# Optimization experiments

Measured on AMD Instinct MI355X. Metric: run time of the kernel, lower is better.

## Reference

```python
import jax, jax.numpy as jnp
import numpy as np


def setup_inputs() -> dict:
    key = jax.random.key(0)
    ks = jax.random.split(key, 6)
    b, t, s, qu, vu, d = 8, 64, 512, 512, 512, 512
    return {
        "query": jax.random.normal(ks[0], (b, t, qu), jnp.float32),
        "value": jax.random.normal(ks[1], (b, s, vu), jnp.float32),
        "mask": jax.random.randint(ks[2], (b, s), 0, 2).astype(bool),
        "W1_w": jax.random.normal(ks[3], (qu, d), jnp.float32) * (1.0 / np.sqrt(qu)),
        "W1_b": jnp.zeros((d,), jnp.float32),
        "W2_w": jax.random.normal(ks[4], (vu, d), jnp.float32) * (1.0 / np.sqrt(vu)),
        "W2_b": jnp.zeros((d,), jnp.float32),
        "scale": jax.random.normal(ks[5], (d,), jnp.float32) * 0.05,
    }


def reference(query, value, mask, W1_w, W1_b, W2_w, W2_b, scale):
    # Dense projections
    q = jnp.einsum('btq,qd->btd', query, W1_w) + W1_b   # [b,t,d]
    k = jnp.einsum('bsv,vd->bsd', value, W2_w) + W2_b   # [b,s,d]
    # Additive (Bahdanau) score with learned scale vector (Keras use_scale=True)
    # scores[b,t,s] = sum_d scale[d] * tanh(q[b,t,d] + k[b,s,d])
    scores = jnp.einsum('btsd,d->bts', jnp.tanh(q[:, :, None, :] + k[:, None, :, :]), scale)
    # Mask over source positions (value mask); query mask is all-ones (no-op)
    scores = jnp.where(mask[:, None, :], scores, jnp.float32(-1e9))
    attention_weights = jax.nn.softmax(scores, axis=-1)   # [b,t,s]
    context_vector = jnp.einsum('bts,bsv->btv', attention_weights, value)  # [b,t,vu]
    return context_vector, attention_weights
```

## Files before the change

kernel.cpp:

```cpp
#include <hip/hip_runtime.h>
#include <hip/hip_bf16.h>

#define B_  8
#define T_  64
#define S_  512
#define D_  512

#define QN (512 * 512)
#define KN (4096 * 512)
#define SN (B_ * T_ * S_)

#define TLOG2E 2.8853900817779268f
#define LOG2E  1.4426950408889634f

typedef __attribute__((ext_vector_type(8))) short bf16x8;
typedef __attribute__((ext_vector_type(4))) float f32x4;

__device__ __forceinline__ unsigned short f2bf(float f) {
    unsigned int u = __float_as_uint(f);
    return (unsigned short)((u + 0x7FFFu + ((u >> 16) & 1u)) >> 16);
}
__device__ __forceinline__ unsigned int pk2(float a, float b) {
    return (unsigned int)f2bf(a) | ((unsigned int)f2bf(b) << 16);
}

__global__ __launch_bounds__(256) void pack_bf16(
    const float* __restrict__ query, const float* __restrict__ value,
    const float* __restrict__ W1, const float* __restrict__ W2,
    unsigned short* __restrict__ qb, unsigned short* __restrict__ vb,
    unsigned short* __restrict__ w1t, unsigned short* __restrict__ w2t)
{
    const int blk = blockIdx.x;
    const int tid = threadIdx.x;
    if (blk < 1152) {
        const float* src; unsigned short* dst; int lb;
        if (blk < 1024) { src = value; dst = vb; lb = blk; }
        else            { src = query; dst = qb; lb = blk - 1024; }
        size_t o = (size_t)lb * 2048 + tid * 8;
        float4 x = *(const float4*)(src + o);
        float4 y = *(const float4*)(src + o + 4);
        uint4 p;
        p.x = pk2(x.x, x.y); p.y = pk2(x.z, x.w);
        p.z = pk2(y.x, y.y); p.w = pk2(y.z, y.w);
        *(uint4*)(dst + o) = p;
    } else {
        const float* W; unsigned short* Wt; int lb;
        if (blk < 1280) { W = W1; Wt = w1t; lb = blk - 1152; }
        else            { W = W2; Wt = w2t; lb = blk - 1280; }
        size_t o = (size_t)lb * 2048 + tid * 8;
        const int n  = (int)(o >> 9);
        const int k0 = (int)(o & 511);
        uint4 p;
        p.x = pk2(W[(size_t)(k0 + 0) * 512 + n], W[(size_t)(k0 + 1) * 512 + n]);
        p.y = pk2(W[(size_t)(k0 + 2) * 512 + n], W[(size_t)(k0 + 3) * 512 + n]);
        p.z = pk2(W[(size_t)(k0 + 4) * 512 + n], W[(size_t)(k0 + 5) * 512 + n]);
        p.w = pk2(W[(size_t)(k0 + 6) * 512 + n], W[(size_t)(k0 + 7) * 512 + n]);
        *(uint4*)(Wt + o) = p;
    }
}

__global__ __launch_bounds__(256) void mfma_gemm(
    const unsigned short* __restrict__ qb, const unsigned short* __restrict__ vb,
    const unsigned short* __restrict__ w1t, const unsigned short* __restrict__ w2t,
    const float* __restrict__ b1, const float* __restrict__ b2,
    float* __restrict__ qproj, float* __restrict__ kproj)
{
    __shared__ __align__(16) unsigned short Ab[64][40];
    __shared__ __align__(16) unsigned short Bb[64][40];

    const int x = blockIdx.x;
    const unsigned short *A, *Bt;
    float* C;
    int tm, tn;
    bool isq;
    if (x < 512) {
        tm = x >> 3; tn = x & 7;
        A = vb; Bt = w2t; C = kproj; isq = false;
    } else {
        int r = x - 512;
        tm = r >> 3; tn = r & 7;
        A = qb; Bt = w1t; C = qproj; isq = true;
    }

    const int tid  = threadIdx.x;
    const int lane = tid & 63;
    const int wid  = tid >> 6;
    const int wm = (wid & 1) * 32, wn = (wid >> 1) * 32;
    const int fm = lane & 15, fq = lane >> 4;

    f32x4 acc00 = {0.f, 0.f, 0.f, 0.f};
    f32x4 acc01 = acc00, acc10 = acc00, acc11 = acc00;

    const int ar = tid >> 2;
    const int ac = (tid & 3) * 8;
    const unsigned short* Ag = A  + (size_t)(tm * 64 + ar) * 512 + ac;
    const unsigned short* Bg = Bt + (size_t)(tn * 64 + ar) * 512 + ac;

    for (int k0 = 0; k0 < 512; k0 += 32) {
        *(uint4*)&Ab[ar][ac] = *(const uint4*)(Ag + k0);
        *(uint4*)&Bb[ar][ac] = *(const uint4*)(Bg + k0);
        __syncthreads();
        bf16x8 a0 = *(const bf16x8*)&Ab[wm + fm][fq * 8];
        bf16x8 a1 = *(const bf16x8*)&Ab[wm + 16 + fm][fq * 8];
        bf16x8 b0 = *(const bf16x8*)&Bb[wn + fm][fq * 8];
        bf16x8 b1v = *(const bf16x8*)&Bb[wn + 16 + fm][fq * 8];
        acc00 = __builtin_amdgcn_mfma_f32_16x16x32_bf16(a0, b0,  acc00, 0, 0, 0);
        acc01 = __builtin_amdgcn_mfma_f32_16x16x32_bf16(a0, b1v, acc01, 0, 0, 0);
        acc10 = __builtin_amdgcn_mfma_f32_16x16x32_bf16(a1, b0,  acc10, 0, 0, 0);
        acc11 = __builtin_amdgcn_mfma_f32_16x16x32_bf16(a1, b1v, acc11, 0, 0, 0);
        __syncthreads();
    }

    const int n0 = tn * 64 + wn + fm;
    const int n1 = n0 + 16;
    float bias0 = 0.f, bias1 = 0.f;
    if (isq) {
        bias0 = b1[n0] + b2[n0];
        bias1 = b1[n1] + b2[n1];
    }
    const int m0 = tm * 64 + wm + fq * 4;
#pragma unroll
    for (int r = 0; r < 4; ++r) {
        C[(size_t)(m0 + r) * 512 + n0]      = (acc00[r] + bias0) * TLOG2E;
        C[(size_t)(m0 + r) * 512 + n1]      = (acc01[r] + bias1) * TLOG2E;
        C[(size_t)(m0 + 16 + r) * 512 + n0] = (acc10[r] + bias0) * TLOG2E;
        C[(size_t)(m0 + 16 + r) * 512 + n1] = (acc11[r] + bias1) * TLOG2E;
    }
}

__global__ __launch_bounds__(256, 4) void scores_t(
    const float* __restrict__ qproj, const float* __restrict__ kproj,
    const int*   __restrict__ mask,  const float* __restrict__ scale,
    float* __restrict__ sparts)
{
    const int blk = blockIdx.x;
    const int b  = blk & 7;
    int r = blk >> 3;
    const int dh = r & 1;
    r >>= 1;
    const int sg = r & 31;
    const int tg = r >> 5;
    const int t0 = tg * 16, s0 = sg * 16;
    const int dbase = dh * 256;

    __shared__ float kT[16][132];
    __shared__ float qT[16][132];
    __shared__ float cS[128];

    const int tid  = threadIdx.x;
    const int t_l = tid >> 4;
    const int s_l = tid & 15;
    const int m = mask[b * S_ + s0 + s_l];

    const int lrow = tid >> 5;
    const int lcol = (tid & 31) * 4;

    float p0 = 0.f, p1 = 0.f;

    for (int c = 0; c < 2; ++c) {
        const int dc = dbase + c * 128;
        const float* kp = kproj + (size_t)(b * S_ + s0) * D_ + dc;
        const float* qp = qproj + (size_t)(b * T_ + t0) * D_ + dc;
        *(float4*)&kT[lrow][lcol]     = *(const float4*)(kp + (size_t)lrow * D_ + lcol);
        *(float4*)&kT[lrow + 8][lcol] = *(const float4*)(kp + (size_t)(lrow + 8) * D_ + lcol);
        *(float4*)&qT[lrow][lcol]     = *(const float4*)(qp + (size_t)lrow * D_ + lcol);
        *(float4*)&qT[lrow + 8][lcol] = *(const float4*)(qp + (size_t)(lrow + 8) * D_ + lcol);
        if (tid < 32) {
            *(float4*)&cS[tid * 4] = *(const float4*)(scale + dc + tid * 4);
        }
        __syncthreads();

#pragma unroll 4
        for (int j = 0; j < 32; ++j) {
            float4 k4 = *(const float4*)&kT[s_l][j * 4];
            float4 q4 = *(const float4*)&qT[t_l][j * 4];
            float4 c4 = *(const float4*)&cS[j * 4];
            float e0 = __builtin_amdgcn_exp2f(q4.x + k4.x);
            float e1 = __builtin_amdgcn_exp2f(q4.y + k4.y);
            float e2 = __builtin_amdgcn_exp2f(q4.z + k4.z);
            float e3 = __builtin_amdgcn_exp2f(q4.w + k4.w);
            float r0 = __builtin_amdgcn_rcpf(e0 + 1.0f);
            float r1 = __builtin_amdgcn_rcpf(e1 + 1.0f);
            float r2 = __builtin_amdgcn_rcpf(e2 + 1.0f);
            float r3 = __builtin_amdgcn_rcpf(e3 + 1.0f);
            p0 = fmaf(c4.x, r0, p0);
            p1 = fmaf(c4.y, r1, p1);
            p0 = fmaf(c4.z, r2, p0);
            p1 = fmaf(c4.w, r3, p1);
        }
        __syncthreads();
    }

    const float p = p0 + p1;
    const float out = m ? (-2.0f * p) : -5e8f;
    sparts[(size_t)dh * SN + (size_t)(b * T_ + t0 + t_l) * S_ + s0 + s_l] = out;
}

__global__ __launch_bounds__(256) void softmax_ctx(
    const float* __restrict__ sparts, const float* __restrict__ value,
    float* __restrict__ ctx, float* __restrict__ attn)
{
    const int blk = blockIdx.x;
    const int b = blk & 7;
    int r = blk >> 3;
    const int vc = r & 3;
    const int tp = r >> 2;
    const int t0 = tp * 2, t1 = t0 + 1;
    const size_t row0 = (size_t)(b * T_ + t0) * S_;
    const size_t row1 = row0 + S_;

    const int tid  = threadIdx.x;
    const int lane = tid & 63;
    const int wid  = tid >> 6;

    __shared__ float2 wp[S_];
    __shared__ float4 part[2][8][32];
    __shared__ float2 red2[8];

    const int sa = tid, sb = tid + 256;
    float2 xa, xb;
    xa.x = sparts[row0 + sa] + sparts[SN + row0 + sa];
    xa.y = sparts[row1 + sa] + sparts[SN + row1 + sa];
    xb.x = sparts[row0 + sb] + sparts[SN + row0 + sb];
    xb.y = sparts[row1 + sb] + sparts[SN + row1 + sb];

    float2 m2; m2.x = fmaxf(xa.x, xb.x); m2.y = fmaxf(xa.y, xb.y);
#pragma unroll
    for (int off = 32; off >= 1; off >>= 1) {
        m2.x = fmaxf(m2.x, __shfl_xor(m2.x, off));
        m2.y = fmaxf(m2.y, __shfl_xor(m2.y, off));
    }
    if (lane == 0) red2[wid] = m2;
    __syncthreads();
    {
        float2 r0 = red2[0], r1 = red2[1], r2 = red2[2], r3 = red2[3];
        m2.x = fmaxf(fmaxf(r0.x, r1.x), fmaxf(r2.x, r3.x));
        m2.y = fmaxf(fmaxf(r0.y, r1.y), fmaxf(r2.y, r3.y));
    }

    float2 ea, eb;
    ea.x = __builtin_amdgcn_exp2f((xa.x - m2.x) * LOG2E);
    ea.y = __builtin_amdgcn_exp2f((xa.y - m2.y) * LOG2E);
    eb.x = __builtin_amdgcn_exp2f((xb.x - m2.x) * LOG2E);
    eb.y = __builtin_amdgcn_exp2f((xb.y - m2.y) * LOG2E);

    float2 s2; s2.x = ea.x + eb.x; s2.y = ea.y + eb.y;
#pragma unroll
    for (int off = 32; off >= 1; off >>= 1) {
        s2.x += __shfl_xor(s2.x, off);
        s2.y += __shfl_xor(s2.y, off);
    }
    if (lane == 0) red2[4 + wid] = s2;
    __syncthreads();
    {
        float2 r0 = red2[4], r1 = red2[5], r2 = red2[6], r3 = red2[7];
        s2.x = (r0.x + r1.x) + (r2.x + r3.x);
        s2.y = (r0.y + r1.y) + (r2.y + r3.y);
    }
    const float inv0 = 1.0f / s2.x, inv1 = 1.0f / s2.y;

    float wa0 = ea.x * inv0, wb0 = eb.x * inv0;
    float wa1 = ea.y * inv1, wb1 = eb.y * inv1;

    float2 wsa; wsa.x = wa0; wsa.y = wa1;
    float2 wsb; wsb.x = wb0; wsb.y = wb1;
    wp[sa] = wsa;
    wp[sb] = wsb;
    if (vc == 0) {
        attn[row0 + sa] = wa0; attn[row0 + sb] = wb0;
        attn[row1 + sa] = wa1; attn[row1 + sb] = wb1;
    }
    __syncthreads();

    const int ssub = wid * 2 + (lane >> 5);
    const int v4   = lane & 31;
    const int v    = vc * 128 + v4 * 4;
    const float* vb = value + ((size_t)(b * S_) + ssub * 64) * D_ + v;
    float4 a0; a0.x = 0.f; a0.y = 0.f; a0.z = 0.f; a0.w = 0.f;
    float4 a1 = a0;
#pragma unroll 4
    for (int i = 0; i < 64; ++i) {
        float4 vv = *(const float4*)(vb + (size_t)i * D_);
        float2 w2 = wp[ssub * 64 + i];
        a0.x = fmaf(w2.x, vv.x, a0.x);
        a0.y = fmaf(w2.x, vv.y, a0.y);
        a0.z = fmaf(w2.x, vv.z, a0.z);
        a0.w = fmaf(w2.x, vv.w, a0.w);
        a1.x = fmaf(w2.y, vv.x, a1.x);
        a1.y = fmaf(w2.y, vv.y, a1.y);
        a1.z = fmaf(w2.y, vv.z, a1.z);
        a1.w = fmaf(w2.y, vv.w, a1.w);
    }
    part[0][ssub][v4] = a0;
    part[1][ssub][v4] = a1;
    __syncthreads();
    if (tid < 64) {
        const int ts = tid >> 5, w4 = tid & 31;
        float4 s0 = part[ts][0][w4], s1 = part[ts][1][w4];
        float4 s2v = part[ts][2][w4], s3 = part[ts][3][w4];
        float4 s4 = part[ts][4][w4], s5 = part[ts][5][w4];
        float4 s6 = part[ts][6][w4], s7 = part[ts][7][w4];
        float4 o;
        o.x = ((s0.x + s1.x) + (s2v.x + s3.x)) + ((s4.x + s5.x) + (s6.x + s7.x));
        o.y = ((s0.y + s1.y) + (s2v.y + s3.y)) + ((s4.y + s5.y) + (s6.y + s7.y));
        o.z = ((s0.z + s1.z) + (s2v.z + s3.z)) + ((s4.z + s5.z) + (s6.z + s7.z));
        o.w = ((s0.w + s1.w) + (s2v.w + s3.w)) + ((s4.w + s5.w) + (s6.w + s7.w));
        *(float4*)(ctx + (size_t)(b * T_ + t0 + ts) * D_ + vc * 128 + w4 * 4) = o;
    }
}

extern "C" void kernel_launch(void* const* d_in, const int* in_sizes, int n_in,
                              void* d_out, int out_size, void* d_ws, size_t ws_size,
                              hipStream_t stream) {
    const float* query = (const float*)d_in[0];
    const float* value = (const float*)d_in[1];
    const int*   mask  = (const int*)  d_in[2];
    const float* W1w   = (const float*)d_in[3];
    const float* W1b   = (const float*)d_in[4];
    const float* W2w   = (const float*)d_in[5];
    const float* W2b   = (const float*)d_in[6];
    const float* scale = (const float*)d_in[7];

    float* ctx  = (float*)d_out;
    float* attn = (float*)d_out + (size_t)B_ * T_ * D_;

    unsigned short* vb  = (unsigned short*)d_ws;
    unsigned short* qb  = vb + (size_t)KN;
    unsigned short* w1t = qb + (size_t)QN;
    unsigned short* w2t = w1t + (size_t)QN;
    float* qproj = (float*)(w2t + (size_t)QN);
    float* kproj = qproj + (size_t)QN;
    float* spart = kproj + (size_t)KN;

    pack_bf16<<<1408, 256, 0, stream>>>(query, value, W1w, W2w, qb, vb, w1t, w2t);
    mfma_gemm<<<576, 256, 0, stream>>>(qb, vb, w1t, w2t, W1b, W2b, qproj, kproj);
    scores_t<<<2048, 256, 0, stream>>>(qproj, kproj, mask, scale, spart);
    softmax_ctx<<<1024, 256, 0, stream>>>(spart, value, ctx, attn);
}
```

Measured before the change: 135.4 us.

## Fuse bf16 packing into GEMM with register prefetch; widen softmax to four rows

```diff
diff --git a/kernel.cpp b/kernel.cpp
--- a/kernel.cpp
+++ b/kernel.cpp
@@ -24,62 +24,28 @@
     return (unsigned int)f2bf(a) | ((unsigned int)f2bf(b) << 16);
 }
 
-__global__ __launch_bounds__(256) void pack_bf16(
+__global__ __launch_bounds__(256) void mfma_gemm(
     const float* __restrict__ query, const float* __restrict__ value,
     const float* __restrict__ W1, const float* __restrict__ W2,
-    unsigned short* __restrict__ qb, unsigned short* __restrict__ vb,
-    unsigned short* __restrict__ w1t, unsigned short* __restrict__ w2t)
-{
-    const int blk = blockIdx.x;
-    const int tid = threadIdx.x;
-    if (blk < 1152) {
-        const float* src; unsigned short* dst; int lb;
-        if (blk < 1024) { src = value; dst = vb; lb = blk; }
-        else            { src = query; dst = qb; lb = blk - 1024; }
-        size_t o = (size_t)lb * 2048 + tid * 8;
-        float4 x = *(const float4*)(src + o);
-        float4 y = *(const float4*)(src + o + 4);
-        uint4 p;
-        p.x = pk2(x.x, x.y); p.y = pk2(x.z, x.w);
-        p.z = pk2(y.x, y.y); p.w = pk2(y.z, y.w);
-        *(uint4*)(dst + o) = p;
-    } else {
-        const float* W; unsigned short* Wt; int lb;
-        if (blk < 1280) { W = W1; Wt = w1t; lb = blk - 1152; }
-        else            { W = W2; Wt = w2t; lb = blk - 1280; }
-        size_t o = (size_t)lb * 2048 + tid * 8;
-        const int n  = (int)(o >> 9);
-        const int k0 = (int)(o & 511);
-        uint4 p;
-        p.x = pk2(W[(size_t)(k0 + 0) * 512 + n], W[(size_t)(k0 + 1) * 512 + n]);
-        p.y = pk2(W[(size_t)(k0 + 2) * 512 + n], W[(size_t)(k0 + 3) * 512 + n]);
-        p.z = pk2(W[(size_t)(k0 + 4) * 512 + n], W[(size_t)(k0 + 5) * 512 + n]);
-        p.w = pk2(W[(size_t)(k0 + 6) * 512 + n], W[(size_t)(k0 + 7) * 512 + n]);
-        *(uint4*)(Wt + o) = p;
-    }
-}
-
-__global__ __launch_bounds__(256) void mfma_gemm(
-    const unsigned short* __restrict__ qb, const unsigned short* __restrict__ vb,
-    const unsigned short* __restrict__ w1t, const unsigned short* __restrict__ w2t,
     const float* __restrict__ b1, const float* __restrict__ b2,
     float* __restrict__ qproj, float* __restrict__ kproj)
 {
     __shared__ __align__(16) unsigned short Ab[64][40];
-    __shared__ __align__(16) unsigned short Bb[64][40];
+    __shared__ __align__(16) unsigned short Bs[64][40];
 
     const int x = blockIdx.x;
-    const unsigned short *A, *Bt;
+    const float *A, *W;
     float* C;
     int tm, tn;
     bool isq;
     if (x < 512) {
-        tm = x >> 3; tn = x & 7;
-        A = vb; Bt = w2t; C = kproj; isq = false;
+        tm = (x & 7) * 8 + ((x >> 3) & 7);
+        tn = x >> 6;
+        A = value; W = W2; C = kproj; isq = false;
     } else {
         int r = x - 512;
         tm = r >> 3; tn = r & 7;
-        A = qb; Bt = w1t; C = qproj; isq = true;
+        A = query; W = W1; C = qproj; isq = true;
     }
 
     const int tid  = threadIdx.x;
@@ -93,22 +59,43 @@
 
     const int ar = tid >> 2;
     const int ac = (tid & 3) * 8;
-    const unsigned short* Ag = A  + (size_t)(tm * 64 + ar) * 512 + ac;
-    const unsigned short* Bg = Bt + (size_t)(tn * 64 + ar) * 512 + ac;
+    const float* Ag = A + (size_t)(tm * 64 + ar) * 512 + ac;
+    const int c0 = (tid & 15) * 4;
+    const int kp = (tid >> 4) * 2;
+    const float* Wg = W + (size_t)kp * 512 + tn * 64 + c0;
+
+    float4 av0 = *(const float4*)(Ag);
+    float4 av1 = *(const float4*)(Ag + 4);
+    float4 wv0 = *(const float4*)(Wg);
+    float4 wv1 = *(const float4*)(Wg + 512);
 
     for (int k0 = 0; k0 < 512; k0 += 32) {
-        *(uint4*)&Ab[ar][ac] = *(const uint4*)(Ag + k0);
-        *(uint4*)&Bb[ar][ac] = *(const uint4*)(Bg + k0);
         __syncthreads();
-        bf16x8 a0 = *(const bf16x8*)&Ab[wm + fm][fq * 8];
-        bf16x8 a1 = *(const bf16x8*)&Ab[wm + 16 + fm][fq * 8];
-        bf16x8 b0 = *(const bf16x8*)&Bb[wn + fm][fq * 8];
-        bf16x8 b1v = *(const bf16x8*)&Bb[wn + 16 + fm][fq * 8];
+        {
+            uint4 pa;
+            pa.x = pk2(av0.x, av0.y); pa.y = pk2(av0.z, av0.w);
+            pa.z = pk2(av1.x, av1.y); pa.w = pk2(av1.z, av1.w);
+            *(uint4*)&Ab[ar][ac] = pa;
+            *(unsigned int*)&Bs[c0 + 0][kp] = pk2(wv0.x, wv1.x);
+            *(unsigned int*)&Bs[c0 + 1][kp] = pk2(wv0.y, wv1.y);
+            *(unsigned int*)&Bs[c0 + 2][kp] = pk2(wv0.z, wv1.z);
+            *(unsigned int*)&Bs[c0 + 3][kp] = pk2(wv0.w, wv1.w);
+        }
+        __syncthreads();
+        const int kn = (k0 + 32) & 511;
+        av0 = *(const float4*)(Ag + kn);
+        av1 = *(const float4*)(Ag + kn + 4);
+        wv0 = *(const float4*)(Wg + (size_t)kn * 512);
+        wv1 = *(const float4*)(Wg + (size_t)kn * 512 + 512);
+
+        bf16x8 a0  = *(const bf16x8*)&Ab[wm + fm][fq * 8];
+        bf16x8 a1  = *(const bf16x8*)&Ab[wm + 16 + fm][fq * 8];
+        bf16x8 b0  = *(const bf16x8*)&Bs[wn + fm][fq * 8];
+        bf16x8 b1v = *(const bf16x8*)&Bs[wn + 16 + fm][fq * 8];
         acc00 = __builtin_amdgcn_mfma_f32_16x16x32_bf16(a0, b0,  acc00, 0, 0, 0);
         acc01 = __builtin_amdgcn_mfma_f32_16x16x32_bf16(a0, b1v, acc01, 0, 0, 0);
         acc10 = __builtin_amdgcn_mfma_f32_16x16x32_bf16(a1, b0,  acc10, 0, 0, 0);
         acc11 = __builtin_amdgcn_mfma_f32_16x16x32_bf16(a1, b1v, acc11, 0, 0, 0);
-        __syncthreads();
     }
 
     const int n0 = tn * 64 + wn + fm;
@@ -204,71 +191,95 @@
     const int b = blk & 7;
     int r = blk >> 3;
     const int vc = r & 3;
-    const int tp = r >> 2;
-    const int t0 = tp * 2, t1 = t0 + 1;
-    const size_t row0 = (size_t)(b * T_ + t0) * S_;
-    const size_t row1 = row0 + S_;
+    const int tq = r >> 2;
+    const int t0 = tq * 4;
+    const size_t rbase = (size_t)(b * T_ + t0) * S_;
 
     const int tid  = threadIdx.x;
     const int lane = tid & 63;
     const int wid  = tid >> 6;
 
-    __shared__ float2 wp[S_];
-    __shared__ float4 part[2][8][32];
-    __shared__ float2 red2[8];
+    __shared__ float4 wp4[S_];
+    __shared__ float4 part[4][8][32];
+    __shared__ float4 red4[8];
 
     const int sa = tid, sb = tid + 256;
-    float2 xa, xb;
-    xa.x = sparts[row0 + sa] + sparts[SN + row0 + sa];
-    xa.y = sparts[row1 + sa] + sparts[SN + row1 + sa];
-    xb.x = sparts[row0 + sb] + sparts[SN + row0 + sb];
-    xb.y = sparts[row1 + sb] + sparts[SN + row1 + sb];
-
-    float2 m2; m2.x = fmaxf(xa.x, xb.x); m2.y = fmaxf(xa.y, xb.y);
+    float4 xa, xb;
+    xa.x = sparts[rbase + sa]          + sparts[SN + rbase + sa];
+    xa.y = sparts[rbase + S_ + sa]     + sparts[SN + rbase + S_ + sa];
+    xa.z = sparts[rbase + 2 * S_ + sa] + sparts[SN + rbase + 2 * S_ + sa];
+    xa.w = sparts[rbase + 3 * S_ + sa] + sparts[SN + rbase + 3 * S_ + sa];
+    xb.x = sparts[rbase + sb]          + sparts[SN + rbase + sb];
+    xb.y = sparts[rbase + S_ + sb]     + sparts[SN + rbase + S_ + sb];
+    xb.z = sparts[rbase + 2 * S_ + sb] + sparts[SN + rbase + 2 * S_ + sb];
+    xb.w = sparts[rbase + 3 * S_ + sb] + sparts[SN + rbase + 3 * S_ + sb];
+
+    float4 m4;
+    m4.x = fmaxf(xa.x, xb.x); m4.y = fmaxf(xa.y, xb.y);
+    m4.z = fmaxf(xa.z, xb.z); m4.w = fmaxf(xa.w, xb.w);
 #pragma unroll
     for (int off = 32; off >= 1; off >>= 1) {
-        m2.x = fmaxf(m2.x, __shfl_xor(m2.x, off));
-        m2.y = fmaxf(m2.y, __shfl_xor(m2.y, off));
-    }
-    if (lane == 0) red2[wid] = m2;
+        m4.x = fmaxf(m4.x, __shfl_xor(m4.x, off));
+        m4.y = fmaxf(m4.y, __shfl_xor(m4.y, off));
+        m4.z = fmaxf(m4.z, __shfl_xor(m4.z, off));
+        m4.w = fmaxf(m4.w, __shfl_xor(m4.w, off));
+    }
+    if (lane == 0) red4[wid] = m4;
     __syncthreads();
     {
-        float2 r0 = red2[0], r1 = red2[1], r2 = red2[2], r3 = red2[3];
-        m2.x = fmaxf(fmaxf(r0.x, r1.x), fmaxf(r2.x, r3.x));
-        m2.y = fmaxf(fmaxf(r0.y, r1.y), fmaxf(r2.y, r3.y));
-    }
-
-    float2 ea, eb;
-    ea.x = __builtin_amdgcn_exp2f((xa.x - m2.x) * LOG2E);
-    ea.y = __builtin_amdgcn_exp2f((xa.y - m2.y) * LOG2E);
-    eb.x = __builtin_amdgcn_exp2f((xb.x - m2.x) * LOG2E);
-    eb.y = __builtin_amdgcn_exp2f((xb.y - m2.y) * LOG2E);
-
-    float2 s2; s2.x = ea.x + eb.x; s2.y = ea.y + eb.y;
+        float4 r0 = red4[0], r1 = red4[1], r2 = red4[2], r3 = red4[3];
+        m4.x = fmaxf(fmaxf(r0.x, r1.x), fmaxf(r2.x, r3.x));
+        m4.y = fmaxf(fmaxf(r0.y, r1.y), fmaxf(r2.y, r3.y));
+        m4.z = fmaxf(fmaxf(r0.z, r1.z), fmaxf(r2.z, r3.z));
+        m4.w = fmaxf(fmaxf(r0.w, r1.w), fmaxf(r2.w, r3.w));
+    }
+
+    float4 ea, eb;
+    ea.x = __builtin_amdgcn_exp2f((xa.x - m4.x) * LOG2E);
+    ea.y = __builtin_amdgcn_exp2f((xa.y - m4.y) * LOG2E);
+    ea.z = __builtin_amdgcn_exp2f((xa.z - m4.z) * LOG2E);
+    ea.w = __builtin_amdgcn_exp2f((xa.w - m4.w) * LOG2E);
+    eb.x = __builtin_amdgcn_exp2f((xb.x - m4.x) * LOG2E);
+    eb.y = __builtin_amdgcn_exp2f((xb.y - m4.y) * LOG2E);
+    eb.z = __builtin_amdgcn_exp2f((xb.z - m4.z) * LOG2E);
+    eb.w = __builtin_amdgcn_exp2f((xb.w - m4.w) * LOG2E);
+
+    float4 s4;
+    s4.x = ea.x + eb.x; s4.y = ea.y + eb.y;
+    s4.z = ea.z + eb.z; s4.w = ea.w + eb.w;
 #pragma unroll
     for (int off = 32; off >= 1; off >>= 1) {
-        s2.x += __shfl_xor(s2.x, off);
-        s2.y += __shfl_xor(s2.y, off);
-    }
-    if (lane == 0) red2[4 + wid] = s2;
+        s4.x += __shfl_xor(s4.x, off);
+        s4.y += __shfl_xor(s4.y, off);
+        s4.z += __shfl_xor(s4.z, off);
+        s4.w += __shfl_xor(s4.w, off);
+    }
+    if (lane == 0) red4[4 + wid] = s4;
     __syncthreads();
     {
-        float2 r0 = red2[4], r1 = red2[5], r2 = red2[6], r3 = red2[7];
-        s2.x = (r0.x + r1.x) + (r2.x + r3.x);
-        s2.y = (r0.y + r1.y) + (r2.y + r3.y);
-    }
-    const float inv0 = 1.0f / s2.x, inv1 = 1.0f / s2.y;
-
-    float wa0 = ea.x * inv0, wb0 = eb.x * inv0;
-    float wa1 = ea.y * inv1, wb1 = eb.y * inv1;
-
-    float2 wsa; wsa.x = wa0; wsa.y = wa1;
-    float2 wsb; wsb.x = wb0; wsb.y = wb1;
-    wp[sa] = wsa;
-    wp[sb] = wsb;
+        float4 r0 = red4[4], r1 = red4[5], r2 = red4[6], r3 = red4[7];
+        s4.x = (r0.x + r1.x) + (r2.x + r3.x);
+        s4.y = (r0.y + r1.y) + (r2.y + r3.y);
+        s4.z = (r0.z + r1.z) + (r2.z + r3.z);
+        s4.w = (r0.w + r1.w) + (r2.w + r3.w);
+    }
+    float4 inv4;
+    inv4.x = 1.0f / s4.x; inv4.y = 1.0f / s4.y;
+    inv4.z = 1.0f / s4.z; inv4.w = 1.0f / s4.w;
+
+    float4 wa, wb;
+    wa.x = ea.x * inv4.x; wa.y = ea.y * inv4.y;
+    wa.z = ea.z * inv4.z; wa.w = ea.w * inv4.w;
+    wb.x = eb.x * inv4.x; wb.y = eb.y * inv4.y;
+    wb.z = eb.z * inv4.z; wb.w = eb.w * inv4.w;
+
+    wp4[sa] = wa;
+    wp4[sb] = wb;
     if (vc == 0) {
-        attn[row0 + sa] = wa0; attn[row0 + sb] = wb0;
-        attn[row1 + sa] = wa1; attn[row1 + sb] = wb1;
+        attn[rbase + sa]          = wa.x; attn[rbase + sb]          = wb.x;
+        attn[rbase + S_ + sa]     = wa.y; attn[rbase + S_ + sb]     = wb.y;
+        attn[rbase + 2 * S_ + sa] = wa.z; attn[rbase + 2 * S_ + sb] = wb.z;
+        attn[rbase + 3 * S_ + sa] = wa.w; attn[rbase + 3 * S_ + sb] = wb.w;
     }
     __syncthreads();
 
@@ -277,35 +288,37 @@
     const int v    = vc * 128 + v4 * 4;
     const float* vb = value + ((size_t)(b * S_) + ssub * 64) * D_ + v;
     float4 a0; a0.x = 0.f; a0.y = 0.f; a0.z = 0.f; a0.w = 0.f;
-    float4 a1 = a0;
+    float4 a1 = a0, a2 = a0, a3 = a0;
 #pragma unroll 4
     for (int i = 0; i < 64; ++i) {
         float4 vv = *(const float4*)(vb + (size_t)i * D_);
-        float2 w2 = wp[ssub * 64 + i];
-        a0.x = fmaf(w2.x, vv.x, a0.x);
-        a0.y = fmaf(w2.x, vv.y, a0.y);
-        a0.z = fmaf(w2.x, vv.z, a0.z);
-        a0.w = fmaf(w2.x, vv.w, a0.w);
-        a1.x = fmaf(w2.y, vv.x, a1.x);
-        a1.y = fmaf(w2.y, vv.y, a1.y);
-        a1.z = fmaf(w2.y, vv.z, a1.z);
-        a1.w = fmaf(w2.y, vv.w, a1.w);
+        float4 w4 = wp4[ssub * 64 + i];
+        a0.x = fmaf(w4.x, vv.x, a0.x); a0.y = fmaf(w4.x, vv.y, a0.y);
+        a0.z = fmaf(w4.x, vv.z, a0.z); a0.w = fmaf(w4.x, vv.w, a0.w);
+        a1.x = fmaf(w4.y, vv.x, a1.x); a1.y = fmaf(w4.y, vv.y, a1.y);
+        a1.z = fmaf(w4.y, vv.z, a1.z); a1.w = fmaf(w4.y, vv.w, a1.w);
+        a2.x = fmaf(w4.z, vv.x, a2.x); a2.y = fmaf(w4.z, vv.y, a2.y);
+        a2.z = fmaf(w4.z, vv.z, a2.z); a2.w = fmaf(w4.z, vv.w, a2.w);
+        a3.x = fmaf(w4.w, vv.x, a3.x); a3.y = fmaf(w4.w, vv.y, a3.y);
+        a3.z = fmaf(w4.w, vv.z, a3.z); a3.w = fmaf(w4.w, vv.w, a3.w);
     }
     part[0][ssub][v4] = a0;
     part[1][ssub][v4] = a1;
+    part[2][ssub][v4] = a2;
+    part[3][ssub][v4] = a3;
     __syncthreads();
-    if (tid < 64) {
-        const int ts = tid >> 5, w4 = tid & 31;
-        float4 s0 = part[ts][0][w4], s1 = part[ts][1][w4];
-        float4 s2v = part[ts][2][w4], s3 = part[ts][3][w4];
-        float4 s4 = part[ts][4][w4], s5 = part[ts][5][w4];
-        float4 s6 = part[ts][6][w4], s7 = part[ts][7][w4];
+    if (tid < 128) {
+        const int ts = tid >> 5, w4i = tid & 31;
+        float4 p0 = part[ts][0][w4i], p1 = part[ts][1][w4i];
+        float4 p2 = part[ts][2][w4i], p3 = part[ts][3][w4i];
+        float4 p4 = part[ts][4][w4i], p5 = part[ts][5][w4i];
+        float4 p6 = part[ts][6][w4i], p7 = part[ts][7][w4i];
         float4 o;
-        o.x = ((s0.x + s1.x) + (s2v.x + s3.x)) + ((s4.x + s5.x) + (s6.x + s7.x));
-        o.y = ((s0.y + s1.y) + (s2v.y + s3.y)) + ((s4.y + s5.y) + (s6.y + s7.y));
-        o.z = ((s0.z + s1.z) + (s2v.z + s3.z)) + ((s4.z + s5.z) + (s6.z + s7.z));
-        o.w = ((s0.w + s1.w) + (s2v.w + s3.w)) + ((s4.w + s5.w) + (s6.w + s7.w));
-        *(float4*)(ctx + (size_t)(b * T_ + t0 + ts) * D_ + vc * 128 + w4 * 4) = o;
+        o.x = ((p0.x + p1.x) + (p2.x + p3.x)) + ((p4.x + p5.x) + (p6.x + p7.x));
+        o.y = ((p0.y + p1.y) + (p2.y + p3.y)) + ((p4.y + p5.y) + (p6.y + p7.y));
+        o.z = ((p0.z + p1.z) + (p2.z + p3.z)) + ((p4.z + p5.z) + (p6.z + p7.z));
+        o.w = ((p0.w + p1.w) + (p2.w + p3.w)) + ((p4.w + p5.w) + (p6.w + p7.w));
+        *(float4*)(ctx + (size_t)(b * T_ + t0 + ts) * D_ + vc * 128 + w4i * 4) = o;
     }
 }
 
@@ -324,16 +337,12 @@
     float* ctx  = (float*)d_out;
     float* attn = (float*)d_out + (size_t)B_ * T_ * D_;
 
-    unsigned short* vb  = (unsigned short*)d_ws;
-    unsigned short* qb  = vb + (size_t)KN;
-    unsigned short* w1t = qb + (size_t)QN;
-    unsigned short* w2t = w1t + (size_t)QN;
-    float* qproj = (float*)(w2t + (size_t)QN);
+    float* qproj = (float*)d_ws;
     float* kproj = qproj + (size_t)QN;
     float* spart = kproj + (size_t)KN;
 
-    pack_bf16<<<1408, 256, 0, stream>>>(query, value, W1w, W2w, qb, vb, w1t, w2t);
-    mfma_gemm<<<576, 256, 0, stream>>>(qb, vb, w1t, w2t, W1b, W2b, qproj, kproj);
+    mfma_gemm<<<576, 256, 0, stream>>>(query, value, W1w, W2w, W1b, W2b,
+                                       qproj, kproj);
     scores_t<<<2048, 256, 0, stream>>>(qproj, kproj, mask, scale, spart);
-    softmax_ctx<<<1024, 256, 0, stream>>>(spart, value, ctx, attn);
-}
+    softmax_ctx<<<512, 256, 0, stream>>>(spart, value, ctx, attn);
+}
```

New measurement: 131.8 us. -2.7%, faster.
